# Performance work log

Measured on AMD Instinct MI355X. Metric: run time of the kernel, lower is better.

## Reference

```python
import jax, jax.numpy as jnp
import numpy as np

B = 16384
IN_DIM = 4096
H1, H2 = 128, 64
LATENT = 32
REPS = 3


def setup_inputs() -> dict:
    key = jax.random.key(0)
    ks = jax.random.split(key, 10)
    def lin(k, fan_in, fan_out):
        bound = 1.0 / np.sqrt(fan_in)
        kw, kb = jax.random.split(k)
        W = jax.random.uniform(kw, (fan_in, fan_out), jnp.float32, -bound, bound)
        b = jax.random.uniform(kb, (fan_out,), jnp.float32, -bound, bound)
        return W, b
    x = jax.random.normal(ks[0], (B, IN_DIM), jnp.float32)
    W1, b1 = lin(ks[1], IN_DIM, H1)
    W2, b2 = lin(ks[2], H1, H2)
    W3, b3 = lin(ks[3], H2, LATENT)
    qparams = jax.random.normal(ks[4], (REPS * 2 * LATENT,), jnp.float32)
    Wd, bd = lin(ks[5], LATENT, IN_DIM)
    return {"x": x, "W1": W1, "b1": b1, "W2": W2, "b2": b2,
            "W3": W3, "b3": b3, "qparams": qparams, "Wd": Wd, "bd": bd}


def _forward(x, W1, b1, W2, b2, W3, b3, qparams, Wd, bd):
    # Classical encoder (dropout inactive in eval mode)
    h = jax.nn.relu(x @ W1 + b1)          # [B, H1]
    h = jax.nn.relu(h @ W2 + b2)          # [B, H2]
    z = h @ W3 + b3                       # [B, LATENT]
    # Quantum decoder: circuit is AngleEmbedding (RX) of latent followed by
    # 2*REPS AngleEmbedding (RX) layers of params -- all RX on the same wire
    # commute and add, no entanglers => <Z_i> = cos(total angle on wire i).
    param_offset = qparams.reshape(2 * REPS, LATENT).sum(axis=0)  # [LATENT]
    q = jnp.cos(z + param_offset)         # [B, LATENT]
    # Classical decoder
    return q @ Wd + bd                    # [B, IN_DIM]


def reference(x, W1, b1, W2, b2, W3, b3, qparams, Wd, bd):
    return _forward(x, W1, b1, W2, b2, W3, b3, qparams, Wd, bd)
```

## Files before the change

### kernel.cpp

```cpp
#include <hip/hip_runtime.h>
#include <hip/hip_bf16.h>

#define B_SZ   16384
#define IN_DIM 4096
#define H1D    128
#define H2D    64
#define LAT    32

typedef _Float16 half8 __attribute__((ext_vector_type(8)));
typedef _Float16 half4 __attribute__((ext_vector_type(4)));
typedef float float4v __attribute__((ext_vector_type(4)));

#define WS_W2T  1048576
#define WS_W3T  1064960
#define WS_WDT  1069056
#define WS_B3O  1331200
#define WS_Q    1331328

__global__ __launch_bounds__(256) void prep_kernel(
    const float* __restrict__ W1, const float* __restrict__ W2,
    const float* __restrict__ W3, const float* __restrict__ Wd,
    const float* __restrict__ b3, const float* __restrict__ qp,
    _Float16* __restrict__ W1t, _Float16* __restrict__ W2t,
    _Float16* __restrict__ W3t, _Float16* __restrict__ Wdt,
    float* __restrict__ b3off)
{
    int t = blockIdx.x * 256 + threadIdx.x;
    if (t < IN_DIM * H1D) {
        int k = t >> 7, n = t & 127;
        W1t[n * IN_DIM + k] = (_Float16)W1[t];
    }
    if (t < LAT * IN_DIM) {
        int k = t >> 12, n = t & 4095;
        Wdt[n * LAT + k] = (_Float16)Wd[t];
    }
    if (t < H1D * H2D) {
        int k = t >> 6, n = t & 63;
        W2t[n * H1D + k] = (_Float16)W2[t];
    }
    if (t < H2D * LAT) {
        int k = t >> 5, n = t & 31;
        W3t[n * H2D + k] = (_Float16)W3[t];
    }
    if (t < LAT) {
        float s = b3[t];
        #pragma unroll
        for (int r = 0; r < 6; ++r) s += qp[r * LAT + t];
        b3off[t] = s;
    }
}

static __device__ __forceinline__ half8 cvt8(float4v v0, float4v v1) {
    half8 h;
    h[0] = (_Float16)v0[0]; h[1] = (_Float16)v0[1];
    h[2] = (_Float16)v0[2]; h[3] = (_Float16)v0[3];
    h[4] = (_Float16)v1[0]; h[5] = (_Float16)v1[1];
    h[6] = (_Float16)v1[2]; h[7] = (_Float16)v1[3];
    return h;
}

__global__ __launch_bounds__(256, 2) void encoder_kernel(
    const float* __restrict__ x,
    const _Float16* __restrict__ W1t, const _Float16* __restrict__ W2t,
    const _Float16* __restrict__ W3t,
    const float* __restrict__ b1, const float* __restrict__ b2,
    const float* __restrict__ b3off, _Float16* __restrict__ qout)
{
    __shared__ alignas(16) float part[4 * 32 * 132];
    __shared__ alignas(16) _Float16 h1s[32 * 136];
    _Float16* h2s = (_Float16*)part;

    const int tid  = threadIdx.x;
    const int lane = tid & 63;
    const int w    = tid >> 6;
    const int l15  = lane & 15;
    const int quad = lane >> 4;
    const int rb0  = blockIdx.x * 32;

    float4v acc[2][8];
    #pragma unroll
    for (int mg = 0; mg < 2; ++mg)
        #pragma unroll
        for (int ct = 0; ct < 8; ++ct)
            acc[mg][ct] = (float4v){0.f, 0.f, 0.f, 0.f};

    const float* xp0 = x + (size_t)(rb0 + l15) * IN_DIM + w * 1024 + quad * 8;
    const float* xp1 = xp0 + 16 * IN_DIM;
    const _Float16* wp[8];
    #pragma unroll
    for (int ct = 0; ct < 8; ++ct)
        wp[ct] = W1t + (size_t)(ct * 16 + l15) * IN_DIM + w * 1024 + quad * 8;

    #pragma unroll 2
    for (int kk = 0; kk < 32; ++kk) {
        const int ko = kk * 32;
        float4v x00 = *(const float4v*)(xp0 + ko);
        float4v x01 = *(const float4v*)(xp0 + ko + 4);
        float4v x10 = *(const float4v*)(xp1 + ko);
        float4v x11 = *(const float4v*)(xp1 + ko + 4);
        half8 a0 = cvt8(x00, x01);
        half8 a1 = cvt8(x10, x11);
        #pragma unroll
        for (int ct = 0; ct < 8; ++ct) {
            half8 b = *(const half8*)(wp[ct] + ko);
            acc[0][ct] = __builtin_amdgcn_mfma_f32_16x16x32_f16(a0, b, acc[0][ct], 0, 0, 0);
            acc[1][ct] = __builtin_amdgcn_mfma_f32_16x16x32_f16(a1, b, acc[1][ct], 0, 0, 0);
        }
    }

    {
        float* pw = part + w * (32 * 132);
        #pragma unroll
        for (int mg = 0; mg < 2; ++mg)
            #pragma unroll
            for (int ct = 0; ct < 8; ++ct)
                #pragma unroll
                for (int r = 0; r < 4; ++r)
                    pw[(mg * 16 + quad * 4 + r) * 132 + ct * 16 + l15] = acc[mg][ct][r];
    }
    __syncthreads();

    #pragma unroll
    for (int i = 0; i < 4; ++i) {
        int chunk = tid * 4 + i;
        int row = chunk >> 5;
        int c4  = chunk & 31;
        const float* p = part + row * 132 + c4 * 4;
        float4v s = *(const float4v*)(p)
                  + *(const float4v*)(p + 32 * 132)
                  + *(const float4v*)(p + 2 * 32 * 132)
                  + *(const float4v*)(p + 3 * 32 * 132);
        float4v bb = *(const float4v*)(b1 + c4 * 4);
        s = s + bb;
        half4 h;
        h[0] = (_Float16)(s[0] > 0.f ? s[0] : 0.f);
        h[1] = (_Float16)(s[1] > 0.f ? s[1] : 0.f);
        h[2] = (_Float16)(s[2] > 0.f ? s[2] : 0.f);
        h[3] = (_Float16)(s[3] > 0.f ? s[3] : 0.f);
        *(half4*)(h1s + row * 136 + c4 * 4) = h;
    }
    __syncthreads();

    {
        float bv2 = b2[w * 16 + l15];
        float4v a2[2] = {(float4v){bv2, bv2, bv2, bv2}, (float4v){bv2, bv2, bv2, bv2}};
        #pragma unroll
        for (int kk = 0; kk < 4; ++kk) {
            half8 b = *(const half8*)(W2t + (w * 16 + l15) * H1D + kk * 32 + quad * 8);
            half8 a0 = *(const half8*)(h1s + l15 * 136 + kk * 32 + quad * 8);
            half8 a1 = *(const half8*)(h1s + (16 + l15) * 136 + kk * 32 + quad * 8);
            a2[0] = __builtin_amdgcn_mfma_f32_16x16x32_f16(a0, b, a2[0], 0, 0, 0);
            a2[1] = __builtin_amdgcn_mfma_f32_16x16x32_f16(a1, b, a2[1], 0, 0, 0);
        }
        __syncthreads();
        #pragma unroll
        for (int mg = 0; mg < 2; ++mg)
            #pragma unroll
            for (int r = 0; r < 4; ++r) {
                float v = a2[mg][r];
                h2s[(mg * 16 + quad * 4 + r) * 72 + w * 16 + l15] = (_Float16)(v > 0.f ? v : 0.f);
            }
    }
    __syncthreads();

    {
        const int mg3 = w >> 1;
        const int ct3 = w & 1;
        const int c3  = ct3 * 16 + l15;
        float bv3 = b3off[c3];
        float4v a3 = (float4v){bv3, bv3, bv3, bv3};
        #pragma unroll
        for (int kk = 0; kk < 2; ++kk) {
            half8 a = *(const half8*)(h2s + (mg3 * 16 + l15) * 72 + kk * 32 + quad * 8);
            half8 b = *(const half8*)(W3t + c3 * H2D + kk * 32 + quad * 8);
            a3 = __builtin_amdgcn_mfma_f32_16x16x32_f16(a, b, a3, 0, 0, 0);
        }
        #pragma unroll
        for (int r = 0; r < 4; ++r) {
            int row = rb0 + mg3 * 16 + quad * 4 + r;
            qout[(size_t)row * LAT + c3] = (_Float16)cosf(a3[r]);
        }
    }
}

__global__ __launch_bounds__(256, 2) void decoder_kernel(
    const _Float16* __restrict__ qin, const _Float16* __restrict__ Wdt,
    const float* __restrict__ bd, float* __restrict__ out)
{
    __shared__ alignas(16) _Float16 qs[64 * 40];
    __shared__ alignas(16) float ot[64 * 260];
    const int tid  = threadIdx.x;
    const int lane = tid & 63;
    const int w    = tid >> 6;
    const int l15  = lane & 15;
    const int quad = lane >> 4;
    const int rowBlk = blockIdx.x >> 4;
    const int colBlk = blockIdx.x & 15;
    const int rb = rowBlk * 64;

    {
        int r = tid >> 2;
        int c = tid & 3;
        uint4 v = *((const uint4*)(qin + (size_t)(rb + r) * LAT) + c);
        *(uint4*)(qs + r * 40 + c * 8) = v;
    }
    __syncthreads();

    half8 a[4];
    #pragma unroll
    for (int mt = 0; mt < 4; ++mt)
        a[mt] = *(const half8*)(qs + (mt * 16 + l15) * 40 + quad * 8);

    #pragma unroll
    for (int nt = 0; nt < 4; ++nt) {
        int ccol = w * 64 + nt * 16 + l15;
        int gcol = colBlk * 256 + ccol;
        half8 b = *(const half8*)(Wdt + (size_t)gcol * LAT + quad * 8);
        float bv = bd[gcol];
        float4v bias = (float4v){bv, bv, bv, bv};
        #pragma unroll
        for (int mt = 0; mt < 4; ++mt) {
            float4v o = __builtin_amdgcn_mfma_f32_16x16x32_f16(a[mt], b, bias, 0, 0, 0);
            #pragma unroll
            for (int r = 0; r < 4; ++r)
                ot[(mt * 16 + quad * 4 + r) * 260 + ccol] = o[r];
        }
    }
    __syncthreads();

    {
        const int trow = tid >> 6;
        const int tcol = (tid & 63) * 4;
        #pragma unroll
        for (int r0 = 0; r0 < 64; r0 += 4) {
            int row = r0 + trow;
            float4v v = *(const float4v*)(ot + row * 260 + tcol);
            *(float4v*)(out + (size_t)(rb + row) * IN_DIM + colBlk * 256 + tcol) = v;
        }
    }
}

extern "C" void kernel_launch(void* const* d_in, const int* in_sizes, int n_in,
                              void* d_out, int out_size, void* d_ws, size_t ws_size,
                              hipStream_t stream)
{
    const float* x  = (const float*)d_in[0];
    const float* W1 = (const float*)d_in[1];
    const float* b1 = (const float*)d_in[2];
    const float* W2 = (const float*)d_in[3];
    const float* b2 = (const float*)d_in[4];
    const float* W3 = (const float*)d_in[5];
    const float* b3 = (const float*)d_in[6];
    const float* qp = (const float*)d_in[7];
    const float* Wd = (const float*)d_in[8];
    const float* bd = (const float*)d_in[9];
    float* out = (float*)d_out;

    char* ws = (char*)d_ws;
    _Float16* W1t = (_Float16*)(ws);
    _Float16* W2t = (_Float16*)(ws + WS_W2T);
    _Float16* W3t = (_Float16*)(ws + WS_W3T);
    _Float16* Wdt = (_Float16*)(ws + WS_WDT);
    float*    b3o = (float*)(ws + WS_B3O);
    _Float16* qbuf= (_Float16*)(ws + WS_Q);

    prep_kernel<<<2048, 256, 0, stream>>>(W1, W2, W3, Wd, b3, qp, W1t, W2t, W3t, Wdt, b3o);
    encoder_kernel<<<512, 256, 0, stream>>>(x, W1t, W2t, W3t, b1, b2, b3o, qbuf);
    decoder_kernel<<<4096, 256, 0, stream>>>(qbuf, Wdt, bd, out);
}
```

Baseline: 519.1 us.

## Fuse decoder into encoder kernel and use nontemporal loads/stores

Removes the separate decoder kernel. Each encoder block now keeps its 32 latent rows in shared memory and computes the full 4096-wide decoder output itself, writing directly to global memory with nontemporal stores. Input x loads also become nontemporal. This drops the q buffer round trip and one launch, but only 512 blocks now do all the output writes, which may limit write parallelism. The transposed MFMA arrangement writes float4 per lane directly and no longer stages output through LDS.

```diff
diff --git a/kernel.cpp b/kernel.cpp
--- a/kernel.cpp
+++ b/kernel.cpp
@@ -15,7 +15,6 @@
 #define WS_W3T  1064960
 #define WS_WDT  1069056
 #define WS_B3O  1331200
-#define WS_Q    1331328
 
 __global__ __launch_bounds__(256) void prep_kernel(
     const float* __restrict__ W1, const float* __restrict__ W2,
@@ -59,16 +58,18 @@
     return h;
 }
 
-__global__ __launch_bounds__(256, 2) void encoder_kernel(
+__global__ __launch_bounds__(256, 2) void fused_kernel(
     const float* __restrict__ x,
     const _Float16* __restrict__ W1t, const _Float16* __restrict__ W2t,
-    const _Float16* __restrict__ W3t,
+    const _Float16* __restrict__ W3t, const _Float16* __restrict__ Wdt,
     const float* __restrict__ b1, const float* __restrict__ b2,
-    const float* __restrict__ b3off, _Float16* __restrict__ qout)
+    const float* __restrict__ b3off, const float* __restrict__ bd,
+    float* __restrict__ out)
 {
     __shared__ alignas(16) float part[4 * 32 * 132];
     __shared__ alignas(16) _Float16 h1s[32 * 136];
     _Float16* h2s = (_Float16*)part;
+    _Float16* qs  = h1s;
 
     const int tid  = threadIdx.x;
     const int lane = tid & 63;
@@ -94,10 +95,10 @@
     #pragma unroll 2
     for (int kk = 0; kk < 32; ++kk) {
         const int ko = kk * 32;
-        float4v x00 = *(const float4v*)(xp0 + ko);
-        float4v x01 = *(const float4v*)(xp0 + ko + 4);
-        float4v x10 = *(const float4v*)(xp1 + ko);
-        float4v x11 = *(const float4v*)(xp1 + ko + 4);
+        float4v x00 = __builtin_nontemporal_load((const float4v*)(xp0 + ko));
+        float4v x01 = __builtin_nontemporal_load((const float4v*)(xp0 + ko + 4));
+        float4v x10 = __builtin_nontemporal_load((const float4v*)(xp1 + ko));
+        float4v x11 = __builtin_nontemporal_load((const float4v*)(xp1 + ko + 4));
         half8 a0 = cvt8(x00, x01);
         half8 a1 = cvt8(x10, x11);
         #pragma unroll
@@ -176,66 +177,27 @@
             a3 = __builtin_amdgcn_mfma_f32_16x16x32_f16(a, b, a3, 0, 0, 0);
         }
         #pragma unroll
-        for (int r = 0; r < 4; ++r) {
-            int row = rb0 + mg3 * 16 + quad * 4 + r;
-            qout[(size_t)row * LAT + c3] = (_Float16)cosf(a3[r]);
-        }
-    }
-}
-
-__global__ __launch_bounds__(256, 2) void decoder_kernel(
-    const _Float16* __restrict__ qin, const _Float16* __restrict__ Wdt,
-    const float* __restrict__ bd, float* __restrict__ out)
-{
-    __shared__ alignas(16) _Float16 qs[64 * 40];
-    __shared__ alignas(16) float ot[64 * 260];
-    const int tid  = threadIdx.x;
-    const int lane = tid & 63;
-    const int w    = tid >> 6;
-    const int l15  = lane & 15;
-    const int quad = lane >> 4;
-    const int rowBlk = blockIdx.x >> 4;
-    const int colBlk = blockIdx.x & 15;
-    const int rb = rowBlk * 64;
-
-    {
-        int r = tid >> 2;
-        int c = tid & 3;
-        uint4 v = *((const uint4*)(qin + (size_t)(rb + r) * LAT) + c);
-        *(uint4*)(qs + r * 40 + c * 8) = v;
-    }
-    __syncthreads();
-
-    half8 a[4];
-    #pragma unroll
-    for (int mt = 0; mt < 4; ++mt)
-        a[mt] = *(const half8*)(qs + (mt * 16 + l15) * 40 + quad * 8);
-
-    #pragma unroll
-    for (int nt = 0; nt < 4; ++nt) {
-        int ccol = w * 64 + nt * 16 + l15;
-        int gcol = colBlk * 256 + ccol;
-        half8 b = *(const half8*)(Wdt + (size_t)gcol * LAT + quad * 8);
-        float bv = bd[gcol];
-        float4v bias = (float4v){bv, bv, bv, bv};
-        #pragma unroll
-        for (int mt = 0; mt < 4; ++mt) {
-            float4v o = __builtin_amdgcn_mfma_f32_16x16x32_f16(a[mt], b, bias, 0, 0, 0);
-            #pragma unroll
-            for (int r = 0; r < 4; ++r)
-                ot[(mt * 16 + quad * 4 + r) * 260 + ccol] = o[r];
-        }
-    }
-    __syncthreads();
-
-    {
-        const int trow = tid >> 6;
-        const int tcol = (tid & 63) * 4;
-        #pragma unroll
-        for (int r0 = 0; r0 < 64; r0 += 4) {
-            int row = r0 + trow;
-            float4v v = *(const float4v*)(ot + row * 260 + tcol);
-            *(float4v*)(out + (size_t)(rb + row) * IN_DIM + colBlk * 256 + tcol) = v;
+        for (int r = 0; r < 4; ++r)
+            qs[(mg3 * 16 + quad * 4 + r) * 40 + c3] = (_Float16)cosf(a3[r]);
+    }
+    __syncthreads();
+
+    {
+        const int wbase = w * 1024;
+        half8 bq0 = *(const half8*)(qs + l15 * 40 + quad * 8);
+        half8 bq1 = *(const half8*)(qs + (16 + l15) * 40 + quad * 8);
+        const _Float16* wdp = Wdt + (size_t)(wbase + l15) * LAT + quad * 8;
+        const float* bdp = bd + wbase + quad * 4;
+        float* op0 = out + (size_t)(rb0 + l15) * IN_DIM + wbase + quad * 4;
+        float* op1 = op0 + (size_t)16 * IN_DIM;
+        #pragma unroll 2
+        for (int ct = 0; ct < 64; ++ct) {
+            half8 aw = *(const half8*)(wdp + ct * 16 * LAT);
+            float4v bias = *(const float4v*)(bdp + ct * 16);
+            float4v o0 = __builtin_amdgcn_mfma_f32_16x16x32_f16(aw, bq0, bias, 0, 0, 0);
+            float4v o1 = __builtin_amdgcn_mfma_f32_16x16x32_f16(aw, bq1, bias, 0, 0, 0);
+            __builtin_nontemporal_store(o0, (float4v*)(op0 + ct * 16));
+            __builtin_nontemporal_store(o1, (float4v*)(op1 + ct * 16));
         }
     }
 }
@@ -262,9 +224,7 @@
     _Float16* W3t = (_Float16*)(ws + WS_W3T);
     _Float16* Wdt = (_Float16*)(ws + WS_WDT);
     float*    b3o = (float*)(ws + WS_B3O);
-    _Float16* qbuf= (_Float16*)(ws + WS_Q);
 
     prep_kernel<<<2048, 256, 0, stream>>>(W1, W2, W3, Wd, b3, qp, W1t, W2t, W3t, Wdt, b3o);
-    encoder_kernel<<<512, 256, 0, stream>>>(x, W1t, W2t, W3t, b1, b2, b3o, qbuf);
-    decoder_kernel<<<4096, 256, 0, stream>>>(qbuf, Wdt, bd, out);
-}
+    fused_kernel<<<512, 256, 0, stream>>>(x, W1t, W2t, W3t, Wdt, b1, b2, b3o, bd, out);
+}
```

Result: slower. 567.8 us (+9.4%).

## Swap MFMA operands in decoder to write output directly without LDS staging

Applied to the files above, without the earlier changes.

The decoder kernel now treats Wd^T tiles as the A operand and the latent q tile as B, so each lane's MFMA result holds four consecutive output columns of one row. Those can be stored straight to global memory as float4, which removes the shared-memory transpose buffer and both barriers. Blocks are reshaped to cover 16 rows by 1024 columns, and launch bounds rise to allow more resident blocks. Each store instruction now covers sixteen rows with 64 bytes each rather than full contiguous rows, which may reduce write coalescing. The launch grid must match the new mapping, and that part is not visible here.

```diff
diff --git a/kernel.cpp b/kernel.cpp
--- a/kernel.cpp
+++ b/kernel.cpp
@@ -183,60 +183,32 @@
     }
 }
 
-__global__ __launch_bounds__(256, 2) void decoder_kernel(
+__global__ __launch_bounds__(256, 8) void decoder_kernel(
     const _Float16* __restrict__ qin, const _Float16* __restrict__ Wdt,
     const float* __restrict__ bd, float* __restrict__ out)
 {
-    __shared__ alignas(16) _Float16 qs[64 * 40];
-    __shared__ alignas(16) float ot[64 * 260];
     const int tid  = threadIdx.x;
     const int lane = tid & 63;
     const int w    = tid >> 6;
     const int l15  = lane & 15;
     const int quad = lane >> 4;
-    const int rowBlk = blockIdx.x >> 4;
-    const int colBlk = blockIdx.x & 15;
-    const int rb = rowBlk * 64;
-
-    {
-        int r = tid >> 2;
-        int c = tid & 3;
-        uint4 v = *((const uint4*)(qin + (size_t)(rb + r) * LAT) + c);
-        *(uint4*)(qs + r * 40 + c * 8) = v;
-    }
-    __syncthreads();
-
-    half8 a[4];
-    #pragma unroll
-    for (int mt = 0; mt < 4; ++mt)
-        a[mt] = *(const half8*)(qs + (mt * 16 + l15) * 40 + quad * 8);
-
-    #pragma unroll
-    for (int nt = 0; nt < 4; ++nt) {
-        int ccol = w * 64 + nt * 16 + l15;
-        int gcol = colBlk * 256 + ccol;
-        half8 b = *(const half8*)(Wdt + (size_t)gcol * LAT + quad * 8);
-        float bv = bd[gcol];
-        float4v bias = (float4v){bv, bv, bv, bv};
-        #pragma unroll
-        for (int mt = 0; mt < 4; ++mt) {
-            float4v o = __builtin_amdgcn_mfma_f32_16x16x32_f16(a[mt], b, bias, 0, 0, 0);
-            #pragma unroll
-            for (int r = 0; r < 4; ++r)
-                ot[(mt * 16 + quad * 4 + r) * 260 + ccol] = o[r];
-        }
-    }
-    __syncthreads();
-
-    {
-        const int trow = tid >> 6;
-        const int tcol = (tid & 63) * 4;
-        #pragma unroll
-        for (int r0 = 0; r0 < 64; r0 += 4) {
-            int row = r0 + trow;
-            float4v v = *(const float4v*)(ot + row * 260 + tcol);
-            *(float4v*)(out + (size_t)(rb + row) * IN_DIM + colBlk * 256 + tcol) = v;
-        }
+    const int stripe   = blockIdx.x >> 2;
+    const int colchunk = blockIdx.x & 3;
+    const int rb    = stripe * 16;
+    const int cbase = colchunk * 1024 + w * 256;
+
+    half8 bq = *(const half8*)(qin + (size_t)(rb + l15) * LAT + quad * 8);
+
+    const _Float16* wdp = Wdt + (size_t)(cbase + l15) * LAT + quad * 8;
+    const float* bdp = bd + cbase + quad * 4;
+    float* op = out + (size_t)(rb + l15) * IN_DIM + cbase + quad * 4;
+
+    #pragma unroll 4
+    for (int ct = 0; ct < 16; ++ct) {
+        half8 aw = *(const half8*)(wdp + ct * 16 * LAT);
+        float4v bias = *(const float4v*)(bdp + ct * 16);
+        float4v o = __builtin_amdgcn_mfma_f32_16x16x32_f16(aw, bq, bias, 0, 0, 0);
+        *(float4v*)(op + ct * 16) = o;
     }
 }
 
```

Measured after the change: 527.7 us. About the same (+1.7%).
